# Performance work log

Measured on AMD Instinct MI355X. Metric: run time of the kernel, lower is better.

Reference implementation:

```python
import jax, jax.numpy as jnp
import numpy as np

B, T, D_MODEL = 2, 2048, 2048
Q_HEADS, KV_HEADS = 16, 4
HEAD_DIM = D_MODEL // Q_HEADS  # 128
N_GROUPS = Q_HEADS // KV_HEADS  # 4
THETA = 10000.0


def setup_inputs() -> dict:
    key = jax.random.key(0)
    ks = jax.random.split(key, 5)
    s = 0.02
    return {
        "x": jax.random.normal(ks[0], (B, T, D_MODEL), dtype=jnp.float32),
        "Wq": jax.random.normal(ks[1], (Q_HEADS * HEAD_DIM, D_MODEL), dtype=jnp.float32) * s,
        "Wk": jax.random.normal(ks[2], (KV_HEADS * HEAD_DIM, D_MODEL), dtype=jnp.float32) * s,
        "Wv": jax.random.normal(ks[3], (KV_HEADS * HEAD_DIM, D_MODEL), dtype=jnp.float32) * s,
        "Wo": jax.random.normal(ks[4], (D_MODEL, D_MODEL), dtype=jnp.float32) * s,
    }


def _apply_rope(q, k, t):
    # freqs = outer(arange(t), 1/theta^(2i/d)) ; complex rotation on (even,odd) pairs
    inv_freq = 1.0 / (THETA ** (jnp.arange(0, HEAD_DIM, 2, dtype=jnp.float32) / HEAD_DIM))
    ang = jnp.arange(t, dtype=jnp.float32)[:, None] * inv_freq[None, :]  # [t, hd/2]
    cos = jnp.cos(ang)[None, :, None, :]  # [1,t,1,hd/2]
    sin = jnp.sin(ang)[None, :, None, :]

    def rot(x):
        xr = x.reshape(*x.shape[:-1], HEAD_DIM // 2, 2)
        xe, xo = xr[..., 0], xr[..., 1]
        out = jnp.stack([xe * cos - xo * sin, xe * sin + xo * cos], axis=-1)
        return out.reshape(x.shape)

    return rot(q), rot(k)


def reference(x, Wq, Wk, Wv, Wo):
    b, t, c = x.shape
    q = (x @ Wq.T).reshape(b, t, Q_HEADS, HEAD_DIM)
    k = (x @ Wk.T).reshape(b, t, KV_HEADS, HEAD_DIM)
    v = (x @ Wv.T).reshape(b, t, KV_HEADS, HEAD_DIM)
    q, k = _apply_rope(q, k, t)
    # GQA: repeat kv heads to match q heads (repeat_interleave on head dim)
    k = jnp.repeat(k, N_GROUPS, axis=2)
    v = jnp.repeat(v, N_GROUPS, axis=2)
    q = q.transpose(0, 2, 1, 3)  # [b,h,t,d]
    k = k.transpose(0, 2, 1, 3)
    v = v.transpose(0, 2, 1, 3)
    scale = HEAD_DIM ** -0.5
    attn = jnp.einsum("bhqd,bhkd->bhqk", q, k) * scale
    causal = jnp.tril(jnp.ones((t, t), dtype=bool))
    attn = jnp.where(causal[None, None], attn, -jnp.inf)
    attn = jax.nn.softmax(attn, axis=-1)
    out = jnp.einsum("bhqk,bhkd->bhqd", attn, v)
    out = out.transpose(0, 2, 1, 3).reshape(b, t, c)
    return out @ Wo.T
```

## Files before the change

### kernel.cpp

```cpp
#include <hip/hip_runtime.h>
#include <hip/hip_bf16.h>

typedef __bf16 bf16_t;
typedef __bf16 bf16x8 __attribute__((ext_vector_type(8)));
typedef __bf16 bf16x4 __attribute__((ext_vector_type(4)));
typedef float f32x4 __attribute__((ext_vector_type(4)));
typedef short short4v __attribute__((ext_vector_type(4)));

#define SEQ_T 2048
#define DMODEL 2048
#define NQH 16
#define NKVH 4
#define HDIM 128

__device__ __forceinline__ f32x4 mfma16x16x32(bf16x8 a, bf16x8 b, f32x4 c) {
  return __builtin_amdgcn_mfma_f32_16x16x32_bf16(a, b, c, 0, 0, 0);
}

typedef __attribute__((address_space(3))) void lds_void_t;
typedef __attribute__((address_space(1))) const void gbl_void_t;
__device__ __forceinline__ void gload_lds16(const bf16_t* g, bf16_t* l) {
  __builtin_amdgcn_global_load_lds((gbl_void_t*)g, (lds_void_t*)l, 16, 0, 0);
}
__device__ __forceinline__ void BAR() {
  asm volatile("" ::: "memory");
  __builtin_amdgcn_s_barrier();
  asm volatile("" ::: "memory");
}

__global__ __launch_bounds__(256) void cast_kernel(const float* __restrict__ src,
                                                   bf16_t* __restrict__ dst, int n8) {
  int idx = blockIdx.x * 256 + threadIdx.x;
  if (idx >= n8) return;
  const float4* s = reinterpret_cast<const float4*>(src) + (size_t)idx * 2;
  float4 a = s[0], b = s[1];
  bf16x8 r = {(bf16_t)a.x, (bf16_t)a.y, (bf16_t)a.z, (bf16_t)a.w,
              (bf16_t)b.x, (bf16_t)b.y, (bf16_t)b.z, (bf16_t)b.w};
  reinterpret_cast<bf16x8*>(dst)[idx] = r;
}

__global__ __launch_bounds__(256) void sincos_kernel(float2* __restrict__ tab) {
  int idx = blockIdx.x * 256 + threadIdx.x;
  int t = idx >> 6, i = idx & 63;
  float inv = powf(10000.0f, -(float)i * (1.0f / 64.0f));
  float ang = (float)t * inv;
  float s, c;
  sincosf(ang, &s, &c);
  tab[idx] = make_float2(c, s);
}

template <int MODE, int BN>
__global__ __launch_bounds__(512, 2) void gemm8p(const bf16_t* __restrict__ A,
                                                 const bf16_t* __restrict__ W,
                                                 bf16_t* __restrict__ q_out,
                                                 bf16_t* __restrict__ k_out,
                                                 bf16_t* __restrict__ v_out,
                                                 float* __restrict__ c_out,
                                                 const float2* __restrict__ tab) {
  constexpr int K = 2048;
  constexpr int NT = K / 64;
  constexpr int NTX = (MODE == 0) ? (3072 / BN) : (2048 / BN);
  constexpr int WN = BN / 4;
  constexpr int NF = WN / 16;
  constexpr int NFH = NF / 2;
  constexpr int NH = 2 + BN / 128;
  const int nwg = gridDim.x;
  const int cpx = nwg >> 3;
  const int id = ((int)blockIdx.x & 7) * cpx + ((int)blockIdx.x >> 3);
  const int m0 = (id / NTX) * 256, n0 = (id % NTX) * BN;
  const int tid = threadIdx.x;
  const int lane = tid & 63, w = tid >> 6;
  const int wr = w >> 2, wc = w & 3;
  const int l15 = lane & 15, g = lane >> 4;
  __shared__ bf16_t smem[2][(256 + BN) * 64];
  f32x4 acc[8][NF] = {};
  bf16x8 af[4][2], bfr[NFH][2];

  auto ISSUE_HALF = [&](int tt, int h) {
    const int k0 = tt * 64;
    bf16_t* base = &smem[tt & 1][0] + ((h < 2) ? h * (128 * 64) : (256 + (h - 2) * 128) * 64);
    const bf16_t* src = (h < 2) ? (A + (size_t)(m0 + h * 128) * K)
                                : (W + (size_t)(n0 + (h - 2) * 128) * K);
#pragma unroll
    for (int i = 0; i < 2; i++) {
      const int rl = i * 64 + (tid >> 3);
      gload_lds16(src + (size_t)rl * K + k0 + (((tid & 7) ^ (rl & 7)) << 3),
                  base + (i * 64 + w * 8) * 64);
    }
  };
  auto RDA = [&](const bf16_t* Ab, int qm) {
#pragma unroll
    for (int fi = 0; fi < 4; fi++) {
      const int row = wr * 128 + qm * 64 + fi * 16 + l15;
#pragma unroll
      for (int ksl = 0; ksl < 2; ksl++)
        af[fi][ksl] = *reinterpret_cast<const bf16x8*>(
            Ab + row * 64 + ((((ksl << 2) + g) ^ (row & 7)) << 3));
    }
  };
  auto RDB = [&](const bf16_t* Bb, int qn) {
#pragma unroll
    for (int fj = 0; fj < NFH; fj++) {
      const int row = wc * WN + qn * (WN / 2) + fj * 16 + l15;
#pragma unroll
      for (int ksl = 0; ksl < 2; ksl++)
        bfr[fj][ksl] = *reinterpret_cast<const bf16x8*>(
            Bb + row * 64 + ((((ksl << 2) + g) ^ (row & 7)) << 3));
    }
  };

#define MMPH(QM, QN)                                                          \
  do {                                                                        \
    __builtin_amdgcn_s_setprio(1);                                            \
    _Pragma("unroll") for (int fi = 0; fi < 4; fi++)                          \
        _Pragma("unroll") for (int fj = 0; fj < NFH; fj++)                    \
            _Pragma("unroll") for (int ksl = 0; ksl < 2; ksl++)               \
                acc[(QM)*4 + fi][(QN)*NFH + fj] = mfma16x16x32(               \
                    af[fi][ksl], bfr[fj][ksl], acc[(QM)*4 + fi][(QN)*NFH + fj]); \
    __builtin_amdgcn_s_setprio(0);                                            \
  } while (0)

#pragma unroll
  for (int h = 0; h < NH; h++) ISSUE_HALF(0, h);

  for (int t = 0; t < NT; t++) {
    const bf16_t* Ab = &smem[t & 1][0];
    const bf16_t* Bb = Ab + 256 * 64;
    if (t + 1 < NT) {
      ISSUE_HALF(t + 1, 0);
      asm volatile("s_waitcnt vmcnt(2)" ::: "memory");
    } else {
      asm volatile("s_waitcnt vmcnt(0)" ::: "memory");
    }
    BAR();
    RDA(Ab, 0);
    RDB(Bb, 0);
    MMPH(0, 0);
    BAR();
    RDB(Bb, 1);
    if (t + 1 < NT) ISSUE_HALF(t + 1, 1);
    BAR();
    MMPH(0, 1);
    BAR();
    RDA(Ab, 1);
    if (t + 1 < NT) ISSUE_HALF(t + 1, 2);
    BAR();
    MMPH(1, 1);
    BAR();
    RDB(Bb, 0);
    if (t + 1 < NT && NH > 3) ISSUE_HALF(t + 1, 3);
    BAR();
    MMPH(1, 0);
    BAR();
  }
#undef MMPH

  if (MODE == 0) {
#pragma unroll
    for (int fm = 0; fm < 8; fm++) {
      const int r0 = m0 + wr * 128 + fm * 16 + (g << 2);
      const int bb = r0 >> 11;
      const int tt = r0 & 2047;
#pragma unroll
      for (int fn = 0; fn < NF; fn++) {
        const int col = n0 + wc * WN + fn * 16 + l15;
        const f32x4 v = acc[fm][fn];
        if (col < 2048) {
          const int dd = col & 127;
          const float2* tp = tab + (size_t)tt * 64 + (dd >> 1);
          bf16_t* dst = q_out + (((size_t)(bb * NQH + (col >> 7)) * SEQ_T + tt) * HDIM + dd);
#pragma unroll
          for (int i = 0; i < 4; i++) {
            float me = v[i];
            float ot = __shfl_xor(me, 1);
            float2 cs = tp[(size_t)i * 64];
            float r = (dd & 1) ? (me * cs.x + ot * cs.y) : (me * cs.x - ot * cs.y);
            dst[(size_t)i * HDIM] = (bf16_t)r;
          }
        } else if (col < 2560) {
          const int dd = col & 127;
          const float2* tp = tab + (size_t)tt * 64 + (dd >> 1);
          bf16_t* dst = k_out + (((size_t)(bb * NKVH + ((col - 2048) >> 7)) * SEQ_T + tt) * HDIM + dd);
#pragma unroll
          for (int i = 0; i < 4; i++) {
            float me = v[i];
            float ot = __shfl_xor(me, 1);
            float2 cs = tp[(size_t)i * 64];
            float r = (dd & 1) ? (me * cs.x + ot * cs.y) : (me * cs.x - ot * cs.y);
            dst[(size_t)i * HDIM] = (bf16_t)r;
          }
        } else {
          const int vc = col - 2560;
          const int hh = vc >> 7, dd = vc & 127;
          const int tp64 = (tt & ~63) | (((tt >> 2) & 3) << 4) | (((tt >> 4) & 3) << 2);
          bf16x4 pk = {(bf16_t)v[0], (bf16_t)v[1], (bf16_t)v[2], (bf16_t)v[3]};
          *reinterpret_cast<bf16x4*>(v_out + (((size_t)(bb * NKVH + hh) * HDIM + dd) * SEQ_T + tp64)) = pk;
        }
      }
    }
  } else {
#pragma unroll
    for (int fm = 0; fm < 8; fm++) {
      const int r0 = m0 + wr * 128 + fm * 16 + (g << 2);
#pragma unroll
      for (int fn = 0; fn < NF; fn++) {
        const int col = n0 + wc * WN + fn * 16 + l15;
#pragma unroll
        for (int i = 0; i < 4; i++) c_out[(size_t)(r0 + i) * 2048 + col] = acc[fm][fn][i];
      }
    }
  }
}

__global__ __launch_bounds__(256, 2) void attn_kernel(const bf16_t* __restrict__ Qb,
                                                      const bf16_t* __restrict__ Kb,
                                                      const bf16_t* __restrict__ Vt,
                                                      bf16_t* __restrict__ AO) {
  const int bh = blockIdx.x;
  const int b = bh >> 4, h = bh & 15, kvh = h >> 2;
  const int p = blockIdx.y;
  const int jH = 31 - p, jL = p;
  const int q0H = jH * 64, q0L = jL * 64;
  const int tid = threadIdx.x;
  const int lane = tid & 63, w = tid >> 6;
  const bf16_t* Qp = Qb + (size_t)(b * NQH + h) * SEQ_T * HDIM;
  const bf16_t* Kp = Kb + (size_t)(b * NKVH + kvh) * SEQ_T * HDIM;
  const bf16_t* Vp = Vt + (size_t)(b * NKVH + kvh) * HDIM * SEQ_T;
  __shared__ bf16_t smem[2][16384];
  const int l15 = lane & 15, g = lane >> 4;
  const int qrA = q0H + w * 16 + l15;
  const int qrB = q0L + w * 16 + l15;
  bf16x8 qfA[4], qfB[4];
#pragma unroll
  for (int c = 0; c < 4; c++) {
    qfA[c] = *reinterpret_cast<const bf16x8*>(Qp + (size_t)qrA * HDIM + c * 32 + (g << 3));
    qfB[c] = *reinterpret_cast<const bf16x8*>(Qp + (size_t)qrB * HDIM + c * 32 + (g << 3));
  }
  f32x4 oA[8] = {}, oB[8] = {};
  float mA = -1e30f, lA = 0.0f, mB = -1e30f, lB = 0.0f;
  const float kscale = 0.08838834764831845f * 1.4426950408889634f;
  const int wmaxB = q0L + w * 16 + 15;
  const int ntiles = jH + 1;

  auto STAGE = [&](int it, int buf) {
    const int kv0s = it * 64;
    bf16_t* Ks = smem[buf];
    bf16_t* Vs = smem[buf] + 8192;
#pragma unroll
    for (int cc = 0; cc < 4; cc++) {
      const int ck = cc * 256 + tid;
      const int krow = ck >> 4, kg = ck & 15;
      gload_lds16(Kp + (size_t)(kv0s + krow) * HDIM + ((kg ^ (krow & 7)) << 3),
                  Ks + (cc * 256 + w * 64) * 8);
      const int vrow = ck >> 3, vg = ck & 7;
      gload_lds16(Vp + (size_t)vrow * SEQ_T + kv0s + ((vg ^ (vrow & 7)) << 3),
                  Vs + (cc * 256 + w * 64) * 8);
    }
  };

  auto SOFTMAX = [&](float* sv, float& m, float& l, f32x4* o, bf16x8* pc) {
    float tm = sv[0];
#pragma unroll
    for (int j = 1; j < 16; j++) tm = fmaxf(tm, sv[j]);
    tm = fmaxf(tm, __shfl_xor(tm, 16, 64));
    tm = fmaxf(tm, __shfl_xor(tm, 32, 64));
    tm *= kscale;
    if (!__all(tm <= m + 8.0f)) {
      const float mnew = fmaxf(m, tm);
      const float alpha = exp2f(m - mnew);
      m = mnew;
      l *= alpha;
#pragma unroll
      for (int dt = 0; dt < 8; dt++) o[dt] *= alpha;
    }
    float rs = 0.0f;
#pragma unroll
    for (int j = 0; j < 16; j++) {
      sv[j] = exp2f(__builtin_fmaf(sv[j], kscale, -m));
      rs += sv[j];
    }
    rs += __shfl_xor(rs, 16, 64);
    rs += __shfl_xor(rs, 32, 64);
    l += rs;
#pragma unroll
    for (int s = 0; s < 2; s++) {
      bf16x8 t = {(bf16_t)sv[8 * s],     (bf16_t)sv[8 * s + 1], (bf16_t)sv[8 * s + 2],
                  (bf16_t)sv[8 * s + 3], (bf16_t)sv[8 * s + 4], (bf16_t)sv[8 * s + 5],
                  (bf16_t)sv[8 * s + 6], (bf16_t)sv[8 * s + 7]};
      pc[s] = t;
    }
  };

  auto COMPUTE1 = [&](const bf16_t* Ks, const bf16_t* Vs, int kv0) {
    float sv[16];
    const bool noMask = (kv0 + 63 <= q0H + w * 16);
    __builtin_amdgcn_s_setprio(1);
#pragma unroll
    for (int ksub = 0; ksub < 4; ksub++) {
      f32x4 sa = {};
      const int krow = ksub * 16 + l15;
#pragma unroll
      for (int ch = 0; ch < 4; ch++) {
        bf16x8 kf = *reinterpret_cast<const bf16x8*>(
            Ks + krow * 128 + ((((ch << 2) + g) ^ (krow & 7)) << 3));
        sa = mfma16x16x32(kf, qfA[ch], sa);
      }
      if (noMask) {
#pragma unroll
        for (int i = 0; i < 4; i++) sv[ksub * 4 + i] = sa[i];
      } else {
        const int dlt = qrA - kv0 - ksub * 16 - (g << 2);
#pragma unroll
        for (int i = 0; i < 4; i++) sv[ksub * 4 + i] = (i <= dlt) ? sa[i] : -3e38f;
      }
    }
    __builtin_amdgcn_s_setprio(0);
    bf16x8 pc[2];
    SOFTMAX(sv, mA, lA, oA, pc);
    __builtin_amdgcn_s_setprio(1);
#pragma unroll
    for (int dt = 0; dt < 8; dt++) {
      const int vrow = dt * 16 + l15;
#pragma unroll
      for (int s = 0; s < 2; s++) {
        bf16x8 vv = *reinterpret_cast<const bf16x8*>(
            Vs + vrow * 64 + (((2 * g + s) ^ (vrow & 7)) << 3));
        oA[dt] = mfma16x16x32(vv, pc[s], oA[dt]);
      }
    }
    __builtin_amdgcn_s_setprio(0);
  };

  auto COMPUTE2 = [&](const bf16_t* Ks, const bf16_t* Vs, int kv0) {
    float svA[16], svB[16];
    const bool noMaskB = (kv0 + 63 <= q0L + w * 16);
    __builtin_amdgcn_s_setprio(1);
#pragma unroll
    for (int ksub = 0; ksub < 4; ksub++) {
      f32x4 sa = {}, sb = {};
      const int krow = ksub * 16 + l15;
#pragma unroll
      for (int ch = 0; ch < 4; ch++) {
        bf16x8 kf = *reinterpret_cast<const bf16x8*>(
            Ks + krow * 128 + ((((ch << 2) + g) ^ (krow & 7)) << 3));
        sa = mfma16x16x32(kf, qfA[ch], sa);
        sb = mfma16x16x32(kf, qfB[ch], sb);
      }
#pragma unroll
      for (int i = 0; i < 4; i++) svA[ksub * 4 + i] = sa[i];
      if (noMaskB) {
#pragma unroll
        for (int i = 0; i < 4; i++) svB[ksub * 4 + i] = sb[i];
      } else {
        const int dltB = qrB - kv0 - ksub * 16 - (g << 2);
#pragma unroll
        for (int i = 0; i < 4; i++) svB[ksub * 4 + i] = (i <= dltB) ? sb[i] : -3e38f;
      }
    }
    __builtin_amdgcn_s_setprio(0);
    bf16x8 pcA[2], pcB[2];
    SOFTMAX(svA, mA, lA, oA, pcA);
    SOFTMAX(svB, mB, lB, oB, pcB);
    __builtin_amdgcn_s_setprio(1);
#pragma unroll
    for (int dt = 0; dt < 8; dt++) {
      const int vrow = dt * 16 + l15;
#pragma unroll
      for (int s = 0; s < 2; s++) {
        bf16x8 vv = *reinterpret_cast<const bf16x8*>(
            Vs + vrow * 64 + (((2 * g + s) ^ (vrow & 7)) << 3));
        oA[dt] = mfma16x16x32(vv, pcA[s], oA[dt]);
        oB[dt] = mfma16x16x32(vv, pcB[s], oB[dt]);
      }
    }
    __builtin_amdgcn_s_setprio(0);
  };

  STAGE(0, 0);
  __syncthreads();
  for (int it = 0; it < ntiles; it++) {
    const int buf = it & 1;
    if (it + 1 < ntiles) STAGE(it + 1, buf ^ 1);
    const int kv0 = it * 64;
    const bf16_t* Ks = smem[buf];
    const bf16_t* Vs = smem[buf] + 8192;
    if (kv0 <= wmaxB) {
      COMPUTE2(Ks, Vs, kv0);
    } else {
      COMPUTE1(Ks, Vs, kv0);
    }
    __syncthreads();
  }
  bf16_t* os = &smem[0][0] + w * 2048;
  auto EPI = [&](f32x4* o, float lsum, int q0) {
    const float linv = 1.0f / lsum;
#pragma unroll
    for (int dt = 0; dt < 8; dt++) {
      bf16x4 pk = {(bf16_t)(o[dt][0] * linv), (bf16_t)(o[dt][1] * linv),
                   (bf16_t)(o[dt][2] * linv), (bf16_t)(o[dt][3] * linv)};
      *reinterpret_cast<bf16x4*>(os + l15 * 128 + dt * 16 + (g << 2)) = pk;
    }
    const size_t rowb = (size_t)b * SEQ_T + q0 + w * 16;
#pragma unroll
    for (int kk = 0; kk < 4; kk++) {
      const int c = lane + kk * 64;
      const int q = c >> 4, gc = c & 15;
      *reinterpret_cast<bf16x8*>(AO + (rowb + q) * DMODEL + h * HDIM + gc * 8) =
          *reinterpret_cast<const bf16x8*>(os + q * 128 + gc * 8);
    }
  };
  EPI(oA, lA, q0H);
  EPI(oB, lB, q0L);
}

extern "C" void kernel_launch(void* const* d_in, const int* in_sizes, int n_in,
                              void* d_out, int out_size, void* d_ws, size_t ws_size,
                              hipStream_t stream) {
  const float* x = (const float*)d_in[0];
  const float* Wq = (const float*)d_in[1];
  const float* Wk = (const float*)d_in[2];
  const float* Wv = (const float*)d_in[3];
  const float* Wo = (const float*)d_in[4];
  float* out = (float*)d_out;
  char* ws = (char*)d_ws;
  bf16_t* xb = (bf16_t*)(ws);
  bf16_t* Wqkvb = (bf16_t*)(ws + 16777216);
  bf16_t* Wob = (bf16_t*)(ws + 29360128);
  bf16_t* Qb = (bf16_t*)(ws + 37748736);
  bf16_t* Kb = (bf16_t*)(ws + 54525952);
  bf16_t* Vt = (bf16_t*)(ws + 58720256);
  bf16_t* AO = (bf16_t*)(ws + 62914560);
  float2* tab = (float2*)(ws + 79691776);

  cast_kernel<<<4096, 256, 0, stream>>>(x, xb, 1048576);
  cast_kernel<<<2048, 256, 0, stream>>>(Wq, Wqkvb, 524288);
  cast_kernel<<<512, 256, 0, stream>>>(Wk, Wqkvb + (size_t)2048 * 2048, 131072);
  cast_kernel<<<512, 256, 0, stream>>>(Wv, Wqkvb + (size_t)2560 * 2048, 131072);
  cast_kernel<<<2048, 256, 0, stream>>>(Wo, Wob, 524288);
  sincos_kernel<<<512, 256, 0, stream>>>(tab);
  gemm8p<0, 256><<<192, 512, 0, stream>>>(xb, Wqkvb, Qb, Kb, Vt, nullptr, tab);
  attn_kernel<<<dim3(32, 16), 256, 0, stream>>>(Qb, Kb, Vt, AO);
  gemm8p<1, 128><<<256, 512, 0, stream>>>(AO, Wob, nullptr, nullptr, nullptr, out, nullptr);
}
```

Before: 192.6 us.

## Fuse cast kernels and retile QKV GEMM to 256x192 tiles over 256 blocks

Merges the five separate fp32-to-bf16 cast launches into one kernel that dispatches on the global index, saving four launches. Specializes the QKV GEMM to a 256x192 tile, so the grid grows from 192 to 256 workgroups and fills the 256 CUs of MI355X instead of leaving some idle. B tiles are now loaded in 64-row chunks, and the MFMA phases are reorganised around three 16-column fragments per wave. The trade-off is a lower per-tile compute-to-load ratio and a different split of memory issue across the pipeline phases.

```diff
diff --git a/kernel.cpp b/kernel.cpp
--- a/kernel.cpp
+++ b/kernel.cpp
@@ -5,7 +5,6 @@
 typedef __bf16 bf16x8 __attribute__((ext_vector_type(8)));
 typedef __bf16 bf16x4 __attribute__((ext_vector_type(4)));
 typedef float f32x4 __attribute__((ext_vector_type(4)));
-typedef short short4v __attribute__((ext_vector_type(4)));
 
 #define SEQ_T 2048
 #define DMODEL 2048
@@ -28,15 +27,42 @@
   asm volatile("" ::: "memory");
 }
 
-__global__ __launch_bounds__(256) void cast_kernel(const float* __restrict__ src,
-                                                   bf16_t* __restrict__ dst, int n8) {
-  int idx = blockIdx.x * 256 + threadIdx.x;
-  if (idx >= n8) return;
-  const float4* s = reinterpret_cast<const float4*>(src) + (size_t)idx * 2;
-  float4 a = s[0], b = s[1];
-  bf16x8 r = {(bf16_t)a.x, (bf16_t)a.y, (bf16_t)a.z, (bf16_t)a.w,
-              (bf16_t)b.x, (bf16_t)b.y, (bf16_t)b.z, (bf16_t)b.w};
-  reinterpret_cast<bf16x8*>(dst)[idx] = r;
+__global__ __launch_bounds__(256) void cast_all(const float* __restrict__ x,
+                                                const float* __restrict__ Wq,
+                                                const float* __restrict__ Wk,
+                                                const float* __restrict__ Wv,
+                                                const float* __restrict__ Wo,
+                                                bf16_t* __restrict__ xb,
+                                                bf16_t* __restrict__ Wqkvb,
+                                                bf16_t* __restrict__ Wob) {
+  const int idx = blockIdx.x * 256 + threadIdx.x;
+  const float* src;
+  bf16_t* dst;
+  if (idx < 1048576) {
+    src = x + (size_t)idx * 8;
+    dst = xb + (size_t)idx * 8;
+  } else if (idx < 1572864) {
+    const int r = idx - 1048576;
+    src = Wq + (size_t)r * 8;
+    dst = Wqkvb + (size_t)r * 8;
+  } else if (idx < 1703936) {
+    const int r = idx - 1572864;
+    src = Wk + (size_t)r * 8;
+    dst = Wqkvb + 4194304 + (size_t)r * 8;
+  } else if (idx < 1835008) {
+    const int r = idx - 1703936;
+    src = Wv + (size_t)r * 8;
+    dst = Wqkvb + 5242880 + (size_t)r * 8;
+  } else {
+    const int r = idx - 1835008;
+    src = Wo + (size_t)r * 8;
+    dst = Wob + (size_t)r * 8;
+  }
+  const float4* s4 = reinterpret_cast<const float4*>(src);
+  float4 a = s4[0], b = s4[1];
+  bf16x8 r8 = {(bf16_t)a.x, (bf16_t)a.y, (bf16_t)a.z, (bf16_t)a.w,
+               (bf16_t)b.x, (bf16_t)b.y, (bf16_t)b.z, (bf16_t)b.w};
+  *reinterpret_cast<bf16x8*>(dst) = r8;
 }
 
 __global__ __launch_bounds__(256) void sincos_kernel(float2* __restrict__ tab) {
@@ -49,38 +75,174 @@
   tab[idx] = make_float2(c, s);
 }
 
-template <int MODE, int BN>
-__global__ __launch_bounds__(512, 2) void gemm8p(const bf16_t* __restrict__ A,
-                                                 const bf16_t* __restrict__ W,
-                                                 bf16_t* __restrict__ q_out,
-                                                 bf16_t* __restrict__ k_out,
-                                                 bf16_t* __restrict__ v_out,
-                                                 float* __restrict__ c_out,
-                                                 const float2* __restrict__ tab) {
+__global__ __launch_bounds__(512, 2) void gemm_qkv(const bf16_t* __restrict__ A,
+                                                   const bf16_t* __restrict__ W,
+                                                   bf16_t* __restrict__ q_out,
+                                                   bf16_t* __restrict__ k_out,
+                                                   bf16_t* __restrict__ v_out,
+                                                   const float2* __restrict__ tab) {
   constexpr int K = 2048;
-  constexpr int NT = K / 64;
-  constexpr int NTX = (MODE == 0) ? (3072 / BN) : (2048 / BN);
-  constexpr int WN = BN / 4;
-  constexpr int NF = WN / 16;
-  constexpr int NFH = NF / 2;
-  constexpr int NH = 2 + BN / 128;
-  const int nwg = gridDim.x;
-  const int cpx = nwg >> 3;
-  const int id = ((int)blockIdx.x & 7) * cpx + ((int)blockIdx.x >> 3);
-  const int m0 = (id / NTX) * 256, n0 = (id % NTX) * BN;
+  constexpr int NT = 32;
+  const int id = ((int)blockIdx.x & 7) * 32 + ((int)blockIdx.x >> 3);
+  const int m0 = (id >> 4) * 256, n0 = (id & 15) * 192;
   const int tid = threadIdx.x;
   const int lane = tid & 63, w = tid >> 6;
   const int wr = w >> 2, wc = w & 3;
   const int l15 = lane & 15, g = lane >> 4;
-  __shared__ bf16_t smem[2][(256 + BN) * 64];
-  f32x4 acc[8][NF] = {};
-  bf16x8 af[4][2], bfr[NFH][2];
+  __shared__ bf16_t smem[2][(256 + 192) * 64];
+  f32x4 acc[8][3] = {};
+  bf16x8 af[4][2], bfr[3][2];
+
+  auto ISSUE_A = [&](int tt, int h) {
+    bf16_t* base = &smem[tt & 1][0] + h * (128 * 64);
+    const bf16_t* src = A + (size_t)(m0 + h * 128) * K + tt * 64;
+#pragma unroll
+    for (int i = 0; i < 2; i++) {
+      const int rl = i * 64 + (tid >> 3);
+      gload_lds16(src + (size_t)rl * K + (((tid & 7) ^ (rl & 7)) << 3),
+                  base + (i * 64 + w * 8) * 64);
+    }
+  };
+  auto ISSUE_B = [&](int tt, int c) {
+    bf16_t* base = &smem[tt & 1][0] + (256 + c * 64) * 64;
+    const int rl = tid >> 3;
+    const bf16_t* src = W + (size_t)(n0 + c * 64 + rl) * K + tt * 64;
+    gload_lds16(src + (((tid & 7) ^ (rl & 7)) << 3), base + (w * 8) * 64);
+  };
+  auto RDA = [&](const bf16_t* Ab, int qm) {
+#pragma unroll
+    for (int fi = 0; fi < 4; fi++) {
+      const int row = wr * 128 + qm * 64 + fi * 16 + l15;
+#pragma unroll
+      for (int ksl = 0; ksl < 2; ksl++)
+        af[fi][ksl] = *reinterpret_cast<const bf16x8*>(
+            Ab + row * 64 + ((((ksl << 2) + g) ^ (row & 7)) << 3));
+    }
+  };
+  auto RDB1 = [&](const bf16_t* Bb, int fj) {
+    const int row = wc * 48 + fj * 16 + l15;
+#pragma unroll
+    for (int ksl = 0; ksl < 2; ksl++)
+      bfr[fj][ksl] = *reinterpret_cast<const bf16x8*>(
+          Bb + row * 64 + ((((ksl << 2) + g) ^ (row & 7)) << 3));
+  };
+
+#define MMX(QM, FJLO, FJHI)                                                   \
+  do {                                                                        \
+    __builtin_amdgcn_s_setprio(1);                                            \
+    _Pragma("unroll") for (int fi = 0; fi < 4; fi++)                          \
+        _Pragma("unroll") for (int fj = (FJLO); fj <= (FJHI); fj++)           \
+            _Pragma("unroll") for (int ksl = 0; ksl < 2; ksl++)               \
+                acc[(QM)*4 + fi][fj] =                                        \
+                    mfma16x16x32(af[fi][ksl], bfr[fj][ksl], acc[(QM)*4 + fi][fj]); \
+    __builtin_amdgcn_s_setprio(0);                                            \
+  } while (0)
+
+  ISSUE_A(0, 0);
+  ISSUE_A(0, 1);
+  ISSUE_B(0, 0);
+  ISSUE_B(0, 1);
+  ISSUE_B(0, 2);
+
+  for (int t = 0; t < NT; t++) {
+    const bf16_t* Ab = &smem[t & 1][0];
+    const bf16_t* Bb = Ab + 256 * 64;
+    if (t + 1 < NT) {
+      ISSUE_A(t + 1, 0);
+      asm volatile("s_waitcnt vmcnt(2)" ::: "memory");
+    } else {
+      asm volatile("s_waitcnt vmcnt(0)" ::: "memory");
+    }
+    BAR();
+    RDA(Ab, 0);
+    RDB1(Bb, 0);
+    RDB1(Bb, 1);
+    MMX(0, 0, 1);
+    BAR();
+    RDB1(Bb, 2);
+    if (t + 1 < NT) ISSUE_A(t + 1, 1);
+    BAR();
+    MMX(0, 2, 2);
+    BAR();
+    RDA(Ab, 1);
+    if (t + 1 < NT) {
+      ISSUE_B(t + 1, 0);
+      ISSUE_B(t + 1, 1);
+    }
+    BAR();
+    MMX(1, 0, 1);
+    BAR();
+    if (t + 1 < NT) ISSUE_B(t + 1, 2);
+    BAR();
+    MMX(1, 2, 2);
+    BAR();
+  }
+#undef MMX
+
+#pragma unroll
+  for (int fm = 0; fm < 8; fm++) {
+    const int r0 = m0 + wr * 128 + fm * 16 + (g << 2);
+    const int bb = r0 >> 11;
+    const int tt = r0 & 2047;
+#pragma unroll
+    for (int fn = 0; fn < 3; fn++) {
+      const int col = n0 + wc * 48 + fn * 16 + l15;
+      const f32x4 v = acc[fm][fn];
+      if (col < 2048) {
+        const int dd = col & 127;
+        const float2* tp = tab + (size_t)tt * 64 + (dd >> 1);
+        bf16_t* dst = q_out + (((size_t)(bb * NQH + (col >> 7)) * SEQ_T + tt) * HDIM + dd);
+#pragma unroll
+        for (int i = 0; i < 4; i++) {
+          float me = v[i];
+          float ot = __shfl_xor(me, 1);
+          float2 cs = tp[(size_t)i * 64];
+          float r = (dd & 1) ? (me * cs.x + ot * cs.y) : (me * cs.x - ot * cs.y);
+          dst[(size_t)i * HDIM] = (bf16_t)r;
+        }
+      } else if (col < 2560) {
+        const int dd = col & 127;
+        const float2* tp = tab + (size_t)tt * 64 + (dd >> 1);
+        bf16_t* dst = k_out + (((size_t)(bb * NKVH + ((col - 2048) >> 7)) * SEQ_T + tt) * HDIM + dd);
+#pragma unroll
+        for (int i = 0; i < 4; i++) {
+          float me = v[i];
+          float ot = __shfl_xor(me, 1);
+          float2 cs = tp[(size_t)i * 64];
+          float r = (dd & 1) ? (me * cs.x + ot * cs.y) : (me * cs.x - ot * cs.y);
+          dst[(size_t)i * HDIM] = (bf16_t)r;
+        }
+      } else {
+        const int vc = col - 2560;
+        const int hh = vc >> 7, dd = vc & 127;
+        const int tp64 = (tt & ~63) | (((tt >> 2) & 3) << 4) | (((tt >> 4) & 3) << 2);
+        bf16x4 pk = {(bf16_t)v[0], (bf16_t)v[1], (bf16_t)v[2], (bf16_t)v[3]};
+        *reinterpret_cast<bf16x4*>(v_out + (((size_t)(bb * NKVH + hh) * HDIM + dd) * SEQ_T + tp64)) = pk;
+      }
+    }
+  }
+}
+
+__global__ __launch_bounds__(512, 2) void gemm_out(const bf16_t* __restrict__ A,
+                                                   const bf16_t* __restrict__ W,
+                                                   float* __restrict__ c_out) {
+  constexpr int K = 2048;
+  constexpr int NT = 32;
+  const int id = ((int)blockIdx.x & 7) * 32 + ((int)blockIdx.x >> 3);
+  const int m0 = (id >> 4) * 256, n0 = (id & 15) * 128;
+  const int tid = threadIdx.x;
+  const int lane = tid & 63, w = tid >> 6;
+  const int wr = w >> 2, wc = w & 3;
+  const int l15 = lane & 15, g = lane >> 4;
+  __shared__ bf16_t smem[2][(256 + 128) * 64];
+  f32x4 acc[8][2] = {};
+  bf16x8 af[4][2], bfr[1][2];
 
   auto ISSUE_HALF = [&](int tt, int h) {
     const int k0 = tt * 64;
-    bf16_t* base = &smem[tt & 1][0] + ((h < 2) ? h * (128 * 64) : (256 + (h - 2) * 128) * 64);
+    bf16_t* base = &smem[tt & 1][0] + ((h < 2) ? h * (128 * 64) : 256 * 64);
     const bf16_t* src = (h < 2) ? (A + (size_t)(m0 + h * 128) * K)
-                                : (W + (size_t)(n0 + (h - 2) * 128) * K);
+                                : (W + (size_t)n0 * K);
 #pragma unroll
     for (int i = 0; i < 2; i++) {
       const int rl = i * 64 + (tid >> 3);
@@ -99,29 +261,25 @@
     }
   };
   auto RDB = [&](const bf16_t* Bb, int qn) {
-#pragma unroll
-    for (int fj = 0; fj < NFH; fj++) {
-      const int row = wc * WN + qn * (WN / 2) + fj * 16 + l15;
-#pragma unroll
-      for (int ksl = 0; ksl < 2; ksl++)
-        bfr[fj][ksl] = *reinterpret_cast<const bf16x8*>(
-            Bb + row * 64 + ((((ksl << 2) + g) ^ (row & 7)) << 3));
-    }
+    const int row = wc * 32 + qn * 16 + l15;
+#pragma unroll
+    for (int ksl = 0; ksl < 2; ksl++)
+      bfr[0][ksl] = *reinterpret_cast<const bf16x8*>(
+          Bb + row * 64 + ((((ksl << 2) + g) ^ (row & 7)) << 3));
   };
 
 #define MMPH(QM, QN)                                                          \
   do {                                                                        \
     __builtin_amdgcn_s_setprio(1);                                            \
     _Pragma("unroll") for (int fi = 0; fi < 4; fi++)                          \
-        _Pragma("unroll") for (int fj = 0; fj < NFH; fj++)                    \
-            _Pragma("unroll") for (int ksl = 0; ksl < 2; ksl++)               \
-                acc[(QM)*4 + fi][(QN)*NFH + fj] = mfma16x16x32(               \
-                    af[fi][ksl], bfr[fj][ksl], acc[(QM)*4 + fi][(QN)*NFH + fj]); \
+        _Pragma("unroll") for (int ksl = 0; ksl < 2; ksl++)                   \
+            acc[(QM)*4 + fi][(QN)] =                                          \
+                mfma16x16x32(af[fi][ksl], bfr[0][ksl], acc[(QM)*4 + fi][(QN)]); \
     __builtin_amdgcn_s_setprio(0);                                            \
   } while (0)
 
 #pragma unroll
-  for (int h = 0; h < NH; h++) ISSUE_HALF(0, h);
+  for (int h = 0; h < 3; h++) ISSUE_HALF(0, h);
 
   for (int t = 0; t < NT; t++) {
     const bf16_t* Ab = &smem[t & 1][0];
@@ -148,66 +306,20 @@
     MMPH(1, 1);
     BAR();
     RDB(Bb, 0);
-    if (t + 1 < NT && NH > 3) ISSUE_HALF(t + 1, 3);
     BAR();
     MMPH(1, 0);
     BAR();
   }
 #undef MMPH
 
-  if (MODE == 0) {
-#pragma unroll
-    for (int fm = 0; fm < 8; fm++) {
-      const int r0 = m0 + wr * 128 + fm * 16 + (g << 2);
-      const int bb = r0 >> 11;
-      const int tt = r0 & 2047;
-#pragma unroll
-      for (int fn = 0; fn < NF; fn++) {
-        const int col = n0 + wc * WN + fn * 16 + l15;
-        const f32x4 v = acc[fm][fn];
-        if (col < 2048) {
-          const int dd = col & 127;
-          const float2* tp = tab + (size_t)tt * 64 + (dd >> 1);
-          bf16_t* dst = q_out + (((size_t)(bb * NQH + (col >> 7)) * SEQ_T + tt) * HDIM + dd);
-#pragma unroll
-          for (int i = 0; i < 4; i++) {
-            float me = v[i];
-            float ot = __shfl_xor(me, 1);
-            float2 cs = tp[(size_t)i * 64];
-            float r = (dd & 1) ? (me * cs.x + ot * cs.y) : (me * cs.x - ot * cs.y);
-            dst[(size_t)i * HDIM] = (bf16_t)r;
-          }
-        } else if (col < 2560) {
-          const int dd = col & 127;
-          const float2* tp = tab + (size_t)tt * 64 + (dd >> 1);
-          bf16_t* dst = k_out + (((size_t)(bb * NKVH + ((col - 2048) >> 7)) * SEQ_T + tt) * HDIM + dd);
-#pragma unroll
-          for (int i = 0; i < 4; i++) {
-            float me = v[i];
-            float ot = __shfl_xor(me, 1);
-            float2 cs = tp[(size_t)i * 64];
-            float r = (dd & 1) ? (me * cs.x + ot * cs.y) : (me * cs.x - ot * cs.y);
-            dst[(size_t)i * HDIM] = (bf16_t)r;
-          }
-        } else {
-          const int vc = col - 2560;
-          const int hh = vc >> 7, dd = vc & 127;
-          const int tp64 = (tt & ~63) | (((tt >> 2) & 3) << 4) | (((tt >> 4) & 3) << 2);
-          bf16x4 pk = {(bf16_t)v[0], (bf16_t)v[1], (bf16_t)v[2], (bf16_t)v[3]};
-          *reinterpret_cast<bf16x4*>(v_out + (((size_t)(bb * NKVH + hh) * HDIM + dd) * SEQ_T + tp64)) = pk;
-        }
-      }
-    }
-  } else {
-#pragma unroll
-    for (int fm = 0; fm < 8; fm++) {
-      const int r0 = m0 + wr * 128 + fm * 16 + (g << 2);
-#pragma unroll
-      for (int fn = 0; fn < NF; fn++) {
-        const int col = n0 + wc * WN + fn * 16 + l15;
-#pragma unroll
-        for (int i = 0; i < 4; i++) c_out[(size_t)(r0 + i) * 2048 + col] = acc[fm][fn][i];
-      }
+#pragma unroll
+  for (int fm = 0; fm < 8; fm++) {
+    const int r0 = m0 + wr * 128 + fm * 16 + (g << 2);
+#pragma unroll
+    for (int fn = 0; fn < 2; fn++) {
+      const int col = n0 + wc * 32 + fn * 16 + l15;
+#pragma unroll
+      for (int i = 0; i < 4; i++) c_out[(size_t)(r0 + i) * 2048 + col] = acc[fm][fn][i];
     }
   }
 }
@@ -432,13 +544,9 @@
   bf16_t* AO = (bf16_t*)(ws + 62914560);
   float2* tab = (float2*)(ws + 79691776);
 
-  cast_kernel<<<4096, 256, 0, stream>>>(x, xb, 1048576);
-  cast_kernel<<<2048, 256, 0, stream>>>(Wq, Wqkvb, 524288);
-  cast_kernel<<<512, 256, 0, stream>>>(Wk, Wqkvb + (size_t)2048 * 2048, 131072);
-  cast_kernel<<<512, 256, 0, stream>>>(Wv, Wqkvb + (size_t)2560 * 2048, 131072);
-  cast_kernel<<<2048, 256, 0, stream>>>(Wo, Wob, 524288);
+  cast_all<<<9216, 256, 0, stream>>>(x, Wq, Wk, Wv, Wo, xb, Wqkvb, Wob);
   sincos_kernel<<<512, 256, 0, stream>>>(tab);
-  gemm8p<0, 256><<<192, 512, 0, stream>>>(xb, Wqkvb, Qb, Kb, Vt, nullptr, tab);
+  gemm_qkv<<<256, 512, 0, stream>>>(xb, Wqkvb, Qb, Kb, Vt, tab);
   attn_kernel<<<dim3(32, 16), 256, 0, stream>>>(Qb, Kb, Vt, AO);
-  gemm8p<1, 128><<<256, 512, 0, stream>>>(AO, Wob, nullptr, nullptr, nullptr, out, nullptr);
-}
+  gemm_out<<<256, 512, 0, stream>>>(AO, Wob, out);
+}
```

Result: faster. 179.6 us (-6.7%).
